# Optimization experiments

Measured on AMD Instinct MI355X. Metric: run time of the kernel, lower is better.

Reference implementation:

```python
import jax, jax.numpy as jnp
import numpy as np

DIM = 64
KSIZE = 3
BN_EPS = 1e-5

def _bn(x):
    # eval-mode BatchNorm2d with default running stats (mean=0, var=1) and affine (1, 0)
    return x / jnp.sqrt(1.0 + BN_EPS)

def _downsample(x, params):
    # four stride-2 3x3 convs: 3 -> 8 -> 16 -> 32 -> 64, BN after each, GELU except after last
    for i, (w, b) in enumerate(params):
        x = jax.lax.conv_general_dilated(x, w, (2, 2), ((1, 1), (1, 1))) + b[None, :, None, None]
        x = _bn(x)
        if i < 3:
            x = jax.nn.gelu(x, approximate=False)
    return x

def _attn(dx, q, kw, kb, vw, vb, pw, pb, dw, db):
    # single-head cross attention: learned queries q (1,T,C) attend to dx (B,N,C)
    scale = DIM ** -0.5
    k = dx @ kw.T + kb
    v = dx @ vw.T + vb
    a = jax.nn.softmax((q @ jnp.swapaxes(k, -1, -2)) * scale, axis=-1)  # (B,T,N)
    o = (a @ v) @ pw.T + pb                                            # (B,T,C)
    return o @ dw.T + db                                               # (B,T,1)

def _gk1d(sigma):
    half = (KSIZE - 1) * 0.5
    x = jnp.linspace(-half, half, KSIZE)
    pdf = jnp.exp(-0.5 * (x / sigma) ** 2)
    return pdf / pdf.sum()

def _gain_denoise(I1, r1, r2, gain, sigma):
    # per-image gain + gaussian-blur unsharp masking, vectorized over the batch
    def one(img, r1i, r2i, gi, si):
        ig = gi * img                                       # (3,H,W)
        k2 = _gk1d(r2i)[:, None] * _gk1d(r1i)[None, :]      # (k,k), sigma_x=r1, sigma_y=r2
        kern = jnp.broadcast_to(k2, (3, 1, KSIZE, KSIZE))   # depthwise kernel
        p = KSIZE // 2
        xp = jnp.pad(ig[None], ((0, 0), (0, 0), (p, p), (p, p)), mode='reflect')
        blur = jax.lax.conv_general_dilated(xp, kern, (1, 1), 'VALID', feature_group_count=3)[0]
        return blur + si * (img - blur)
    return jax.vmap(one)(I1, r1, r2, gain, sigma)

def setup_inputs():
    key = jax.random.key(0)
    ks = iter(jax.random.split(key, 64))
    def rn(shape, s=0.05):
        return jax.random.normal(next(ks), shape, dtype=jnp.float32) * s
    def ru(shape):
        return jax.random.uniform(next(ks), shape, dtype=jnp.float32)
    inp = {"I1": ru((8, 3, 512, 512))}
    for pre, T in (("kp", 4), ("mp", 10)):
        inp[pre + "_q"] = ru((1, T, DIM))
        chans = [3, DIM // 8, DIM // 4, DIM // 2, DIM]
        for i in range(4):
            inp[pre + "_c%dw" % (i + 1)] = rn((chans[i + 1], chans[i], 3, 3), 0.1)
            inp[pre + "_c%db" % (i + 1)] = jnp.zeros((chans[i + 1],), jnp.float32)
        for nm, shp in (("kw", (DIM, DIM)), ("vw", (DIM, DIM)), ("pw", (DIM, DIM)), ("dw", (1, DIM))):
            inp[pre + "_" + nm] = rn(shp)
        for nm, n in (("kb", DIM), ("vb", DIM), ("pb", DIM), ("db", 1)):
            inp[pre + "_" + nm] = jnp.zeros((n,), jnp.float32)
    inp["kp_gain_base"] = jnp.ones((1,), jnp.float32)  # mode='normal'
    dims = [3, 32, 32, 32, 32, 3]
    for i in range(5):
        inp["lut_w%d" % i] = rn((dims[i + 1], dims[i]), 0.2)
        inp["lut_b%d" % i] = jnp.zeros((dims[i + 1],), jnp.float32)
    return inp

def reference(I1, kp_q, kp_c1w, kp_c1b, kp_c2w, kp_c2b, kp_c3w, kp_c3b, kp_c4w, kp_c4b,
              kp_kw, kp_kb, kp_vw, kp_vb, kp_pw, kp_pb, kp_dw, kp_db, kp_gain_base,
              mp_q, mp_c1w, mp_c1b, mp_c2w, mp_c2b, mp_c3w, mp_c3b, mp_c4w, mp_c4b,
              mp_kw, mp_kb, mp_vw, mp_vb, mp_pw, mp_pb, mp_dw, mp_db,
              lut_w0, lut_b0, lut_w1, lut_b1, lut_w2, lut_b2, lut_w3, lut_b3, lut_w4, lut_b4):
    B = I1.shape[0]
    # --- Kernel_Predictor ---
    dx = _downsample(I1, [(kp_c1w, kp_c1b), (kp_c2w, kp_c2b), (kp_c3w, kp_c3b), (kp_c4w, kp_c4b)])
    dx = dx.reshape(B, DIM, -1).transpose(0, 2, 1)            # (B,N,C), N=(H/16)*(W/16)
    o = _attn(dx, kp_q, kp_kw, kp_kb, kp_vw, kp_vb, kp_pw, kp_pb, kp_dw, kp_db)[..., 0]  # (B,4)
    r1 = 0.1 * o[:, 0] + 3.0
    r2 = 0.1 * o[:, 1] + 2.0
    gain = o[:, 2] + kp_gain_base[0]
    sigma = jax.nn.sigmoid(o[:, 3])
    # --- gain + gaussian unsharp denoise ---
    I2 = jnp.clip(_gain_denoise(I1, r1, r2, gain, sigma), 1e-5, 1.0)
    # --- Matrix_Predictor ---
    dx2 = _downsample(I2, [(mp_c1w, mp_c1b), (mp_c2w, mp_c2b), (mp_c3w, mp_c3b), (mp_c4w, mp_c4b)])
    dx2 = dx2.reshape(B, DIM, -1).transpose(0, 2, 1)
    o2 = _attn(dx2, mp_q, mp_kw, mp_kb, mp_vw, mp_vb, mp_pw, mp_pb, mp_dw, mp_db)  # (B,10,1)
    ccm = 0.1 * o2[:, :9, 0].reshape(B, 3, 3) + jnp.eye(3, dtype=I1.dtype)
    dist = jax.nn.relu(o2[:, 9, 0]) + 1.0                     # (B,)
    # --- Shades-of-Gray white balance + CCM ---
    hwc = I2.transpose(0, 2, 3, 1)                            # (B,H,W,3)
    imgP = hwc ** dist[:, None, None, None]
    ch = jnp.mean(imgP, axis=(1, 2)) ** (1.0 / dist)[:, None]  # (B,3)
    avg = jnp.mean(imgP, axis=(1, 2, 3)) ** (1.0 / dist)       # (B,)
    I3 = hwc / (ch / avg[:, None])[:, None, None, :]
    I4 = jnp.clip(jnp.einsum('bhwc,bdc->bhwd', I3, ccm), 1e-5, 1.0)
    # --- NILUT residual per-pixel MLP ---
    h = jax.nn.relu(I4 @ lut_w0.T + lut_b0)
    h = jnp.tanh(h @ lut_w1.T + lut_b1)
    h = jnp.tanh(h @ lut_w2.T + lut_b2)
    h = jnp.tanh(h @ lut_w3.T + lut_b3)
    I5 = jnp.clip(h @ lut_w4.T + lut_b4 + I4, 0.0, 1.0)
    return I5.transpose(0, 3, 1, 2)                           # (B,3,H,W)
```

## Files before the change

kernel.cpp:

```cpp
#include <hip/hip_runtime.h>
#include <math.h>


#define BN_MUL 0.9999950000374997f

static constexpr int BB   = 8;
static constexpr int HH   = 512;
static constexpr int WW   = 512;
static constexpr int HW   = HH * WW;
static constexpr int NTOK = 1024;
static constexpr int DIMC = 64;
static constexpr int WBCH = 32;

typedef _Float16 f16x8 __attribute__((ext_vector_type(8)));
typedef _Float16 f16x2 __attribute__((ext_vector_type(2)));
typedef float    f32x4 __attribute__((ext_vector_type(4)));

__device__ __forceinline__ float gelu_exact(float x) {
    return 0.5f * x * (1.0f + erff(x * 0.7071067811865476f));
}

__device__ __forceinline__ float tanh_fast(float x) {
    float e = __expf(2.0f * x);
    return 1.0f - 2.0f * __builtin_amdgcn_rcpf(e + 1.0f);
}

template<int Cin, int Hin, int OCT, bool GELU>
__global__ __launch_bounds__(256) void conv_s2(const float* __restrict__ in,
                                               const float* __restrict__ wt,
                                               const float* __restrict__ bs,
                                               float* __restrict__ out)
{
    constexpr int Win  = Hin, Hout = Hin / 2, Wout = Hin / 2;
    constexpr int WSH  = (Wout == 256) ? 8 : (Wout == 128) ? 7 : (Wout == 64) ? 6 : 5;
    constexpr int PLANE = Hout * Wout;

    const int sp  = blockIdx.x * 256 + threadIdx.x;
    const int ow  = sp & (Wout - 1);
    const int oh  = sp >> WSH;
    const int oc0 = blockIdx.y * OCT;
    const int b   = blockIdx.z;
    const int Cout = (int)gridDim.y * OCT;

    float acc[OCT];
    #pragma unroll
    for (int o = 0; o < OCT; ++o) acc[o] = bs[oc0 + o];

    const int ih0 = oh * 2 - 1, iw0 = ow * 2 - 1;
    const float fh0 = (ih0 >= 0) ? 1.f : 0.f;
    const float fw0 = (iw0 >= 0) ? 1.f : 0.f;
    const int r0 = (ih0 >= 0) ? ih0 : 0;
    const int cc0 = (iw0 >= 0) ? iw0 : 0;

    const float* ip = in + (size_t)(b * Cin) * Hin * Win;
    #pragma unroll
    for (int ic = 0; ic < Cin; ++ic) {
        const float* pl = ip + ic * Hin * Win;
        const float* p0 = pl + r0 * Win;
        const float* p1 = pl + (ih0 + 1) * Win;
        const float* p2 = pl + (ih0 + 2) * Win;
        float  v00 = p0[cc0] * (fh0 * fw0);
        float2 va  = *(const float2*)(p0 + iw0 + 1);
        float  v01 = va.x * fh0, v02 = va.y * fh0;
        float  v10 = p1[cc0] * fw0;
        float2 vb  = *(const float2*)(p1 + iw0 + 1);
        float  v20 = p2[cc0] * fw0;
        float2 vc  = *(const float2*)(p2 + iw0 + 1);
        #pragma unroll
        for (int o = 0; o < OCT; ++o) {
            const float* wr = wt + ((oc0 + o) * Cin + ic) * 9;
            acc[o] += v00 * wr[0] + v01 * wr[1] + v02 * wr[2]
                    + v10 * wr[3] + vb.x * wr[4] + vb.y * wr[5]
                    + v20 * wr[6] + vc.x * wr[7] + vc.y * wr[8];
        }
    }
    #pragma unroll
    for (int o = 0; o < OCT; ++o) {
        float a = acc[o] * BN_MUL;
        if (GELU) a = gelu_exact(a);
        out[(size_t)(b * Cout + oc0 + o) * PLANE + sp] = a;
    }
}

__global__ __launch_bounds__(256) void denoise_conv1_kernel(
    const float* __restrict__ I1, const float* __restrict__ attno,
    const float* __restrict__ gain_base,
    const float* __restrict__ wt, const float* __restrict__ bs,
    float* __restrict__ I2, float* __restrict__ out)
{
    const int sp = blockIdx.x * 256 + threadIdx.x;
    const int ow = sp & 255;
    const int oh = sp >> 8;
    const int b  = blockIdx.z;

    const float o0 = attno[b * 4 + 0], o1 = attno[b * 4 + 1];
    const float o2 = attno[b * 4 + 2], o3 = attno[b * 4 + 3];
    const float r1 = 0.1f * o0 + 3.0f;
    const float r2 = 0.1f * o1 + 2.0f;
    const float g  = o2 + gain_base[0];
    const float sg = 1.0f / (1.0f + __expf(-o3));
    const float ex = __expf(-0.5f / (r1 * r1));
    const float nx = 1.0f / (2.0f * ex + 1.0f);
    const float ey = __expf(-0.5f / (r2 * r2));
    const float ny = 1.0f / (2.0f * ey + 1.0f);
    const float kx0 = ex * nx, kx1 = nx;
    const float ky0 = ey * ny, ky1 = ny;

    const int rbase = 2 * oh - 2, cbase = 2 * ow - 2;
    int ri[5], ci[5];
    #pragma unroll
    for (int i = 0; i < 5; ++i) {
        int r = rbase + i; ri[i] = r < 0 ? -r : (r > 511 ? 1022 - r : r);
        int c = cbase + i; ci[i] = c < 0 ? -c : (c > 511 ? 1022 - c : c);
    }
    const bool topE = (oh == 0), leftE = (ow == 0);

    float acc[8];
    #pragma unroll
    for (int o = 0; o < 8; ++o) acc[o] = bs[o];

    #pragma unroll
    for (int c = 0; c < 3; ++c) {
        const float* ip = I1 + ((size_t)b * 3 + c) * HW;
        float p[5][5];
        #pragma unroll
        for (int i = 0; i < 5; ++i) {
            const float* rp = ip + ri[i] * WW;
            #pragma unroll
            for (int j = 0; j < 5; ++j) p[i][j] = rp[ci[j]];
        }
        float hs[5][3];
        #pragma unroll
        for (int i = 0; i < 5; ++i)
            #pragma unroll
            for (int j = 0; j < 3; ++j)
                hs[i][j] = kx0 * (p[i][j] + p[i][j + 2]) + kx1 * p[i][j + 1];
        float w2[3][3];
        #pragma unroll
        for (int i = 0; i < 3; ++i)
            #pragma unroll
            for (int j = 0; j < 3; ++j) {
                float bl = g * (ky0 * (hs[i][j] + hs[i + 2][j]) + ky1 * hs[i + 1][j]);
                float val = bl + sg * (p[i + 1][j + 1] - bl);
                w2[i][j] = fminf(fmaxf(val, 1e-5f), 1.0f);
            }
        float* op = I2 + ((size_t)b * 3 + c) * HW + (2 * oh) * WW + 2 * ow;
        float2 w0v; w0v.x = w2[1][1]; w0v.y = w2[1][2];
        float2 w1v; w1v.x = w2[2][1]; w1v.y = w2[2][2];
        *(float2*)op        = w0v;
        *(float2*)(op + WW) = w1v;
        if (topE)  { w2[0][0] = 0.f; w2[0][1] = 0.f; w2[0][2] = 0.f; }
        if (leftE) { w2[0][0] = 0.f; w2[1][0] = 0.f; w2[2][0] = 0.f; }
        #pragma unroll
        for (int o = 0; o < 8; ++o) {
            const float* wr = wt + (o * 3 + c) * 9;
            acc[o] += w2[0][0] * wr[0] + w2[0][1] * wr[1] + w2[0][2] * wr[2]
                    + w2[1][0] * wr[3] + w2[1][1] * wr[4] + w2[1][2] * wr[5]
                    + w2[2][0] * wr[6] + w2[2][1] * wr[7] + w2[2][2] * wr[8];
        }
    }
    #pragma unroll
    for (int o = 0; o < 8; ++o)
        out[(b * 8 + o) * 65536 + sp] = gelu_exact(acc[o] * BN_MUL);
}

__global__ __launch_bounds__(1024) void attn_kernel(
    const float* __restrict__ dx, const float* __restrict__ q,
    const float* __restrict__ kw, const float* __restrict__ kb,
    const float* __restrict__ vw, const float* __restrict__ vb,
    const float* __restrict__ pw, const float* __restrict__ pb,
    const float* __restrict__ dw, const float* __restrict__ db,
    float* __restrict__ outv, int T)
{
    __shared__ float qk[DIMC];
    __shared__ float red[1024];
    __shared__ float sc[NTOK];
    __shared__ float uN[DIMC];
    __shared__ float osh[DIMC];
    __shared__ float psh[DIMC];
    __shared__ float qkb_s;
    const int tid = threadIdx.x;
    const int bt  = blockIdx.x;
    const int b = bt / T, t = bt - b * T;
    const float* qt = q + t * DIMC;

    if (tid < DIMC) {
        float s = 0.f;
        #pragma unroll
        for (int c = 0; c < DIMC; ++c) s += qt[c] * kw[c * DIMC + tid];
        qk[tid] = s;
    }
    if (tid == 1023) {
        float s = 0.f;
        #pragma unroll
        for (int c = 0; c < DIMC; ++c) s += qt[c] * kb[c];
        qkb_s = s;
    }
    __syncthreads();

    const float* dp = dx + (size_t)(b * DIMC) * NTOK;
    float s = qkb_s;
    #pragma unroll
    for (int c = 0; c < DIMC; ++c) s += qk[c] * dp[c * NTOK + tid];
    s *= 0.125f;

    red[tid] = s;
    __syncthreads();
    for (int off = 512; off > 0; off >>= 1) {
        if (tid < off) red[tid] = fmaxf(red[tid], red[tid + off]);
        __syncthreads();
    }
    float m = red[0];
    __syncthreads();

    float e = __expf(s - m);
    sc[tid] = e;
    red[tid] = e;
    __syncthreads();
    for (int off = 512; off > 0; off >>= 1) {
        if (tid < off) red[tid] += red[tid + off];
        __syncthreads();
    }
    float Ssum = red[0];
    __syncthreads();

    const int c  = tid & 63, qq = tid >> 6;
    float part = 0.f;
    const float* dr = dp + c * NTOK + qq * 64;
    const float* sr = sc + qq * 64;
    #pragma unroll
    for (int n = 0; n < 64; ++n) part += sr[n] * dr[n];
    red[tid] = part;
    __syncthreads();
    if (tid < DIMC) {
        float u = 0.f;
        #pragma unroll
        for (int k = 0; k < 16; ++k) u += red[tid + k * 64];
        uN[tid] = u / Ssum;
    }
    __syncthreads();
    if (tid < DIMC) {
        float o = vb[tid];
        const float* vr = vw + tid * DIMC;
        #pragma unroll
        for (int cc = 0; cc < DIMC; ++cc) o += vr[cc] * uN[cc];
        osh[tid] = o;
    }
    __syncthreads();
    if (tid < DIMC) {
        float p = pb[tid];
        const float* pr = pw + tid * DIMC;
        #pragma unroll
        for (int cc = 0; cc < DIMC; ++cc) p += pr[cc] * osh[cc];
        psh[tid] = p;
    }
    __syncthreads();
    if (tid == 0) {
        float r = db[0];
        #pragma unroll
        for (int cc = 0; cc < DIMC; ++cc) r += psh[cc] * dw[cc];
        outv[bt] = r;
    }
}

__global__ __launch_bounds__(256) void wb_reduce_kernel(const float* __restrict__ I2,
                                                        const float* __restrict__ attno,
                                                        float* __restrict__ part)
{
    __shared__ float red[256];
    const int bc = blockIdx.y;
    const int b  = bc / 3;
    float d = attno[b * 10 + 9];
    d = fmaxf(d, 0.f) + 1.0f;
    constexpr int CHUNK = HW / WBCH;
    const float4* base = (const float4*)(I2 + (size_t)bc * HW + blockIdx.x * CHUNK);
    float l = 0.f;
    #pragma unroll
    for (int i = threadIdx.x, it = 0; it < CHUNK / 4 / 256; ++it, i += 256) {
        float4 v = base[i];
        l += __expf(d * __logf(v.x)) + __expf(d * __logf(v.y))
           + __expf(d * __logf(v.z)) + __expf(d * __logf(v.w));
    }
    red[threadIdx.x] = l;
    __syncthreads();
    for (int off = 128; off > 0; off >>= 1) {
        if (threadIdx.x < off) red[threadIdx.x] += red[threadIdx.x + off];
        __syncthreads();
    }
    if (threadIdx.x == 0) part[bc * WBCH + blockIdx.x] = red[0];
}

__global__ void wb_finalize_kernel(const float* __restrict__ part,
                                   const float* __restrict__ attno,
                                   float* __restrict__ wbsc)
{
    int b = threadIdx.x;
    if (b >= BB) return;
    float d = attno[b * 10 + 9];
    d = fmaxf(d, 0.f) + 1.0f;
    float inv = 1.0f / d;
    float s[3];
    #pragma unroll
    for (int c = 0; c < 3; ++c) {
        float t0 = 0.f;
        const float* pp = part + (b * 3 + c) * WBCH;
        #pragma unroll
        for (int k = 0; k < WBCH; ++k) t0 += pp[k];
        s[c] = t0;
    }
    float avg = powf((s[0] + s[1] + s[2]) / (3.0f * (float)HW), inv);
    #pragma unroll
    for (int c = 0; c < 3; ++c)
        wbsc[b * 4 + c] = avg / powf(s[c] / (float)HW, inv);
}

__global__ void __launch_bounds__(256) final_kernel(
    float* __restrict__ io,
    const float* __restrict__ wbsc, const float* __restrict__ attno,
    const float* __restrict__ w0, const float* __restrict__ b0,
    const float* __restrict__ w1, const float* __restrict__ b1,
    const float* __restrict__ w2, const float* __restrict__ b2,
    const float* __restrict__ w3, const float* __restrict__ b3,
    const float* __restrict__ w4, const float* __restrict__ b4)
{
    constexpr int ROW = 72;
    __shared__ __align__(16) _Float16 LDS[4][64 * ROW];
    const int tid  = threadIdx.x;
    const int wv   = tid >> 6;
    const int lane = tid & 63;
    const int nn   = lane & 15;
    const int quad = lane >> 4;
    _Float16* Wl = LDS[wv];

    const int b   = blockIdx.x >> 10;
    const int pix = (blockIdx.x * 256 + tid) & (HW - 1);
    float* base = io + b * 3 * HW + pix;

    const float s0 = wbsc[b * 4 + 0], s1 = wbsc[b * 4 + 1], s2 = wbsc[b * 4 + 2];
    float v0 = base[0] * s0;
    float v1 = base[HW] * s1;
    float v2 = base[2 * HW] * s2;
    const float* o2p = attno + b * 10;
    float I4[3];
    #pragma unroll
    for (int d = 0; d < 3; ++d) {
        float m0 = 0.1f * o2p[d * 3]     + (d == 0 ? 1.f : 0.f);
        float m1 = 0.1f * o2p[d * 3 + 1] + (d == 1 ? 1.f : 0.f);
        float m2 = 0.1f * o2p[d * 3 + 2] + (d == 2 ? 1.f : 0.f);
        I4[d] = fminf(fmaxf(m0 * v0 + m1 * v1 + m2 * v2, 1e-5f), 1.0f);
    }

    #pragma unroll
    for (int j = 0; j < 32; j += 2) {
        float a0 = b0[j]   + w0[j*3]     * I4[0] + w0[j*3+1]     * I4[1] + w0[j*3+2]     * I4[2];
        float a1 = b0[j+1] + w0[(j+1)*3] * I4[0] + w0[(j+1)*3+1] * I4[1] + w0[(j+1)*3+2] * I4[2];
        f16x2 p;
        p[0] = (_Float16)fmaxf(a0, 0.f);
        p[1] = (_Float16)fmaxf(a1, 0.f);
        *(f16x2*)&Wl[lane * ROW + j] = p;
    }

    f16x8 wf[3][2];
    float bv[3][2];
    const float* wls[3] = { w1, w2, w3 };
    const float* bls[3] = { b1, b2, b3 };
    #pragma unroll
    for (int L = 0; L < 3; ++L) {
        #pragma unroll
        for (int h = 0; h < 2; ++h) {
            const float* wr = wls[L] + (16 * h + nn) * 32 + quad * 8;
            #pragma unroll
            for (int i = 0; i < 8; ++i) wf[L][h][i] = (_Float16)wr[i];
            bv[L][h] = bls[L][16 * h + nn];
        }
    }
    __syncthreads();

    #pragma unroll
    for (int L = 0; L < 3; ++L) {
        f16x8 af[4];
        #pragma unroll
        for (int t = 0; t < 4; ++t)
            af[t] = *(const f16x8*)&Wl[(16 * t + nn) * ROW + quad * 8];
        __syncthreads();
        #pragma unroll
        for (int t = 0; t < 4; ++t) {
            #pragma unroll
            for (int h = 0; h < 2; ++h) {
                f32x4 c;
                c[0] = c[1] = c[2] = c[3] = bv[L][h];
                f32x4 d = __builtin_amdgcn_mfma_f32_16x16x32_f16(af[t], wf[L][h], c, 0, 0, 0);
                #pragma unroll
                for (int r = 0; r < 4; ++r)
                    Wl[(16 * t + quad * 4 + r) * ROW + 16 * h + nn] = (_Float16)tanh_fast(d[r]);
            }
        }
        __syncthreads();
    }

    float h4[32];
    #pragma unroll
    for (int g = 0; g < 4; ++g) {
        f16x8 rv = *(const f16x8*)&Wl[lane * ROW + g * 8];
        #pragma unroll
        for (int i = 0; i < 8; ++i) h4[g * 8 + i] = (float)rv[i];
    }
    #pragma unroll
    for (int d = 0; d < 3; ++d) {
        float a = b4[d];
        const float* wr = w4 + d * 32;
        #pragma unroll
        for (int k = 0; k < 32; ++k) a += h4[k] * wr[k];
        a += I4[d];
        base[d * HW] = fminf(fmaxf(a, 0.f), 1.0f);
    }
}

extern "C" void kernel_launch(void* const* d_in, const int* in_sizes, int n_in,
                              void* d_out, int out_size, void* d_ws, size_t ws_size,
                              hipStream_t stream)
{
    const float* I1      = (const float*)d_in[0];
    const float* kp_q    = (const float*)d_in[1];
    const float* kp_c1w  = (const float*)d_in[2];  const float* kp_c1b = (const float*)d_in[3];
    const float* kp_c2w  = (const float*)d_in[4];  const float* kp_c2b = (const float*)d_in[5];
    const float* kp_c3w  = (const float*)d_in[6];  const float* kp_c3b = (const float*)d_in[7];
    const float* kp_c4w  = (const float*)d_in[8];  const float* kp_c4b = (const float*)d_in[9];
    const float* kp_kw   = (const float*)d_in[10]; const float* kp_vw  = (const float*)d_in[11];
    const float* kp_pw   = (const float*)d_in[12]; const float* kp_dw  = (const float*)d_in[13];
    const float* kp_kb   = (const float*)d_in[14]; const float* kp_vb  = (const float*)d_in[15];
    const float* kp_pb   = (const float*)d_in[16]; const float* kp_db  = (const float*)d_in[17];
    const float* mp_q    = (const float*)d_in[18];
    const float* mp_c1w  = (const float*)d_in[19]; const float* mp_c1b = (const float*)d_in[20];
    const float* mp_c2w  = (const float*)d_in[21]; const float* mp_c2b = (const float*)d_in[22];
    const float* mp_c3w  = (const float*)d_in[23]; const float* mp_c3b = (const float*)d_in[24];
    const float* mp_c4w  = (const float*)d_in[25]; const float* mp_c4b = (const float*)d_in[26];
    const float* mp_kw   = (const float*)d_in[27]; const float* mp_vw  = (const float*)d_in[28];
    const float* mp_pw   = (const float*)d_in[29]; const float* mp_dw  = (const float*)d_in[30];
    const float* mp_kb   = (const float*)d_in[31]; const float* mp_vb  = (const float*)d_in[32];
    const float* mp_pb   = (const float*)d_in[33]; const float* mp_db  = (const float*)d_in[34];
    const float* gainb   = (const float*)d_in[35];
    const float* lw0 = (const float*)d_in[36]; const float* lb0 = (const float*)d_in[37];
    const float* lw1 = (const float*)d_in[38]; const float* lb1 = (const float*)d_in[39];
    const float* lw2 = (const float*)d_in[40]; const float* lb2 = (const float*)d_in[41];
    const float* lw3 = (const float*)d_in[42]; const float* lb3 = (const float*)d_in[43];
    const float* lw4 = (const float*)d_in[44]; const float* lb4 = (const float*)d_in[45];

    float* ws    = (float*)d_ws;
    float* ds1   = ws;
    float* ds2   = ds1 + 8 * 8 * 256 * 256;
    float* ds3   = ds2 + 8 * 16 * 128 * 128;
    float* ds4   = ds3 + 8 * 32 * 64 * 64;
    float* attno = ds4 + 8 * 64 * 32 * 32;
    float* part  = attno + 128;
    float* wbsc  = part + 24 * WBCH;
    float* I2    = (float*)d_out;

    conv_s2<3, 512, 8, true ><<<dim3(256, 1, BB), 256, 0, stream>>>(I1,  kp_c1w, kp_c1b, ds1);
    conv_s2<8, 256, 8, true ><<<dim3(64,  2, BB), 256, 0, stream>>>(ds1, kp_c2w, kp_c2b, ds2);
    conv_s2<16, 128, 4, true><<<dim3(16,  8, BB), 256, 0, stream>>>(ds2, kp_c3w, kp_c3b, ds3);
    conv_s2<32, 64, 4, false><<<dim3(4,  16, BB), 256, 0, stream>>>(ds3, kp_c4w, kp_c4b, ds4);
    attn_kernel<<<BB * 4, 1024, 0, stream>>>(ds4, kp_q, kp_kw, kp_kb, kp_vw, kp_vb,
                                             kp_pw, kp_pb, kp_dw, kp_db, attno, 4);

    denoise_conv1_kernel<<<dim3(256, 1, BB), 256, 0, stream>>>(I1, attno, gainb,
                                                               mp_c1w, mp_c1b, I2, ds1);

    conv_s2<8, 256, 8, true ><<<dim3(64,  2, BB), 256, 0, stream>>>(ds1, mp_c2w, mp_c2b, ds2);
    conv_s2<16, 128, 4, true><<<dim3(16,  8, BB), 256, 0, stream>>>(ds2, mp_c3w, mp_c3b, ds3);
    conv_s2<32, 64, 4, false><<<dim3(4,  16, BB), 256, 0, stream>>>(ds3, mp_c4w, mp_c4b, ds4);
    attn_kernel<<<BB * 10, 1024, 0, stream>>>(ds4, mp_q, mp_kw, mp_kb, mp_vw, mp_vb,
                                              mp_pw, mp_pb, mp_dw, mp_db, attno, 10);

    wb_reduce_kernel<<<dim3(WBCH, 24), 256, 0, stream>>>(I2, attno, part);
    wb_finalize_kernel<<<1, 64, 0, stream>>>(part, attno, wbsc);

    final_kernel<<<BB * HW / 256, 256, 0, stream>>>(I2, wbsc, attno,
        lw0, lb0, lw1, lb1, lw2, lb2, lw3, lb3, lw4, lb4);
}
```

Measured before the change: 435.2 us.

## Precompute fp16 MLP weights and drop block barriers in per-pixel LUT kernel

```diff
diff --git a/kernel.cpp b/kernel.cpp
--- a/kernel.cpp
+++ b/kernel.cpp
@@ -292,38 +292,49 @@
 
 __global__ void wb_finalize_kernel(const float* __restrict__ part,
                                    const float* __restrict__ attno,
-                                   float* __restrict__ wbsc)
-{
-    int b = threadIdx.x;
-    if (b >= BB) return;
-    float d = attno[b * 10 + 9];
-    d = fmaxf(d, 0.f) + 1.0f;
-    float inv = 1.0f / d;
-    float s[3];
-    #pragma unroll
-    for (int c = 0; c < 3; ++c) {
-        float t0 = 0.f;
-        const float* pp = part + (b * 3 + c) * WBCH;
-        #pragma unroll
-        for (int k = 0; k < WBCH; ++k) t0 += pp[k];
-        s[c] = t0;
-    }
-    float avg = powf((s[0] + s[1] + s[2]) / (3.0f * (float)HW), inv);
-    #pragma unroll
-    for (int c = 0; c < 3; ++c)
-        wbsc[b * 4 + c] = avg / powf(s[c] / (float)HW, inv);
+                                   float* __restrict__ wbsc,
+                                   const float* __restrict__ w1,
+                                   const float* __restrict__ w2,
+                                   const float* __restrict__ w3,
+                                   _Float16* __restrict__ whf)
+{
+    const int t = threadIdx.x;
+    for (int i = t; i < 1024; i += 256) {
+        whf[i]        = (_Float16)w1[i];
+        whf[1024 + i] = (_Float16)w2[i];
+        whf[2048 + i] = (_Float16)w3[i];
+    }
+    if (t < BB) {
+        const int b = t;
+        float d = attno[b * 10 + 9];
+        d = fmaxf(d, 0.f) + 1.0f;
+        float inv = 1.0f / d;
+        float s[3];
+        #pragma unroll
+        for (int c = 0; c < 3; ++c) {
+            float t0 = 0.f;
+            const float* pp = part + (b * 3 + c) * WBCH;
+            #pragma unroll
+            for (int k = 0; k < WBCH; ++k) t0 += pp[k];
+            s[c] = t0;
+        }
+        float avg = powf((s[0] + s[1] + s[2]) / (3.0f * (float)HW), inv);
+        #pragma unroll
+        for (int c = 0; c < 3; ++c)
+            wbsc[b * 4 + c] = avg / powf(s[c] / (float)HW, inv);
+    }
 }
 
 __global__ void __launch_bounds__(256) final_kernel(
     float* __restrict__ io,
     const float* __restrict__ wbsc, const float* __restrict__ attno,
+    const _Float16* __restrict__ whf,
     const float* __restrict__ w0, const float* __restrict__ b0,
-    const float* __restrict__ w1, const float* __restrict__ b1,
-    const float* __restrict__ w2, const float* __restrict__ b2,
-    const float* __restrict__ w3, const float* __restrict__ b3,
+    const float* __restrict__ b1, const float* __restrict__ b2,
+    const float* __restrict__ b3,
     const float* __restrict__ w4, const float* __restrict__ b4)
 {
-    constexpr int ROW = 72;
+    constexpr int ROW = 40;
     __shared__ __align__(16) _Float16 LDS[4][64 * ROW];
     const int tid  = threadIdx.x;
     const int wv   = tid >> 6;
@@ -362,19 +373,17 @@
 
     f16x8 wf[3][2];
     float bv[3][2];
-    const float* wls[3] = { w1, w2, w3 };
     const float* bls[3] = { b1, b2, b3 };
     #pragma unroll
     for (int L = 0; L < 3; ++L) {
         #pragma unroll
         for (int h = 0; h < 2; ++h) {
-            const float* wr = wls[L] + (16 * h + nn) * 32 + quad * 8;
-            #pragma unroll
-            for (int i = 0; i < 8; ++i) wf[L][h][i] = (_Float16)wr[i];
+            wf[L][h] = *(const f16x8*)&whf[L * 1024 + (16 * h + nn) * 32 + quad * 8];
             bv[L][h] = bls[L][16 * h + nn];
         }
     }
-    __syncthreads();
+    asm volatile("s_waitcnt lgkmcnt(0)" ::: "memory");
+    __builtin_amdgcn_sched_barrier(0);
 
     #pragma unroll
     for (int L = 0; L < 3; ++L) {
@@ -382,20 +391,22 @@
         #pragma unroll
         for (int t = 0; t < 4; ++t)
             af[t] = *(const f16x8*)&Wl[(16 * t + nn) * ROW + quad * 8];
-        __syncthreads();
-        #pragma unroll
-        for (int t = 0; t < 4; ++t) {
+        asm volatile("s_waitcnt lgkmcnt(0)" ::: "memory");
+        __builtin_amdgcn_sched_barrier(0);
+        #pragma unroll
+        for (int h = 0; h < 2; ++h) {
+            f32x4 cb;
+            cb[0] = cb[1] = cb[2] = cb[3] = bv[L][h];
             #pragma unroll
-            for (int h = 0; h < 2; ++h) {
-                f32x4 c;
-                c[0] = c[1] = c[2] = c[3] = bv[L][h];
-                f32x4 d = __builtin_amdgcn_mfma_f32_16x16x32_f16(af[t], wf[L][h], c, 0, 0, 0);
+            for (int t = 0; t < 4; ++t) {
+                f32x4 d = __builtin_amdgcn_mfma_f32_16x16x32_f16(af[t], wf[L][h], cb, 0, 0, 0);
                 #pragma unroll
                 for (int r = 0; r < 4; ++r)
                     Wl[(16 * t + quad * 4 + r) * ROW + 16 * h + nn] = (_Float16)tanh_fast(d[r]);
             }
         }
-        __syncthreads();
+        asm volatile("s_waitcnt lgkmcnt(0)" ::: "memory");
+        __builtin_amdgcn_sched_barrier(0);
     }
 
     float h4[32];
@@ -455,6 +466,7 @@
     float* part  = attno + 128;
     float* wbsc  = part + 24 * WBCH;
     float* I2    = (float*)d_out;
+    _Float16* whf = (_Float16*)ds1;
 
     conv_s2<3, 512, 8, true ><<<dim3(256, 1, BB), 256, 0, stream>>>(I1,  kp_c1w, kp_c1b, ds1);
     conv_s2<8, 256, 8, true ><<<dim3(64,  2, BB), 256, 0, stream>>>(ds1, kp_c2w, kp_c2b, ds2);
@@ -473,8 +485,8 @@
                                               mp_pw, mp_pb, mp_dw, mp_db, attno, 10);
 
     wb_reduce_kernel<<<dim3(WBCH, 24), 256, 0, stream>>>(I2, attno, part);
-    wb_finalize_kernel<<<1, 64, 0, stream>>>(part, attno, wbsc);
-
-    final_kernel<<<BB * HW / 256, 256, 0, stream>>>(I2, wbsc, attno,
-        lw0, lb0, lw1, lb1, lw2, lb2, lw3, lb3, lw4, lb4);
-}
+    wb_finalize_kernel<<<1, 256, 0, stream>>>(part, attno, wbsc, lw1, lw2, lw3, whf);
+
+    final_kernel<<<BB * HW / 256, 256, 0, stream>>>(I2, wbsc, attno, whf,
+        lw0, lb0, lb1, lb2, lb3, lw4, lb4);
+}
```

New measurement: 431.6 us. No clear change (-0.8%).
